# Kernel optimization log

Hardware: AMD Instinct MI355X
Metric: run time of the kernel (lower is better)

The kernel has to match this reference:

```python
import jax, jax.numpy as jnp
import numpy as np

N_QUBITS = 8  # 2**8 == hidden_dim == 256


def setup_inputs() -> dict:
    key = jax.random.key(0)
    ks = jax.random.split(key, 6)
    B, H, F = 131072, 256, 512
    s = lambda fan: 1.0 / np.sqrt(fan)
    return {
        "x": jax.random.normal(ks[0], (B, N_QUBITS), jnp.float32),
        "W1": jax.random.normal(ks[1], (N_QUBITS, H), jnp.float32) * s(N_QUBITS),
        "b1": jnp.zeros((H,), jnp.float32),
        "W2": jax.random.normal(ks[2], (H, H), jnp.float32) * s(H),
        "b2": jnp.zeros((H,), jnp.float32),
        "W3": jax.random.normal(ks[3], (H, H), jnp.float32) * s(H),
        "b3": jnp.zeros((H,), jnp.float32),
        "W4": jax.random.normal(ks[4], (H, F), jnp.float32) * s(H),
        "b4": jnp.zeros((F,), jnp.float32),
    }


def _quantum_state(enc):
    # Ry(theta_i) on qubit i from |0...0>: product state, amplitudes are
    # kron_i [cos(theta_i/2), sin(theta_i/2)] (real). Qubit 0 = most significant.
    half = enc[:, :N_QUBITS] * (jnp.pi / 2)  # theta/2 = enc*pi/2
    amps = jnp.stack([jnp.cos(half), jnp.sin(half)], axis=-1)  # [B, n, 2]
    B = enc.shape[0]
    state = jnp.ones((B, 1), enc.dtype)
    for i in range(N_QUBITS):  # fixed small structural loop
        state = (state[:, :, None] * amps[:, i, None, :]).reshape(B, -1)
    return state  # [B, 2**n]


def reference(x, W1, b1, W2, b2, W3, b3, W4, b4):
    h = jax.nn.relu(x @ W1 + b1)
    enc = jax.nn.relu(h @ W2 + b2)           # [B, 256]
    state = _quantum_state(enc)              # [B, 256]
    f = jax.nn.relu(state @ W3 + b3)
    return f @ W4 + b4                       # [B, 512]
```

## Files before the change

### kernel.cpp

```cpp
#include <hip/hip_runtime.h>
#include <hip/hip_bf16.h>

typedef short s8v __attribute__((ext_vector_type(8)));
typedef float f4v __attribute__((ext_vector_type(4)));
typedef unsigned short u16;
typedef unsigned int u32;

#define PI_HALF 1.57079632679489662f

__global__ void prep_kernel(const float* __restrict__ W1,
                            const float* __restrict__ W2,
                            const float* __restrict__ W3,
                            const float* __restrict__ W4,
                            u16* __restrict__ w3f,
                            u16* __restrict__ w4f,
                            float* __restrict__ w1t,
                            float* __restrict__ w2c) {
  int i = blockIdx.x * 256 + threadIdx.x;
  if (i < 65536) {
    int j = i & 7, lane = (i >> 3) & 63, kk = (i >> 9) & 7, ntg = i >> 12;
    int k = kk * 32 + (lane >> 4) * 8 + j;
    int n = ntg * 16 + (lane & 15);
    __hip_bfloat16 v = __float2bfloat16(W3[k * 256 + n]);
    w3f[i] = *(u16*)&v;
  } else if (i < 65536 + 131072) {
    int t = i - 65536;
    int j = t & 7, lane = (t >> 3) & 63, kk = (t >> 9) & 7, ntg = t >> 12;
    int k = kk * 32 + (lane >> 4) * 8 + j;
    int n = ntg * 16 + (lane & 15);
    __hip_bfloat16 v = __float2bfloat16(W4[k * 512 + n]);
    w4f[t] = *(u16*)&v;
  } else if (i < 65536 + 131072 + 2048) {
    int t = i - (65536 + 131072);
    int k = t >> 3, j = t & 7;
    w1t[t] = W1[j * 256 + k];
  } else if (i < 65536 + 131072 + 4096) {
    int t = i - (65536 + 131072 + 2048);
    int k = t >> 3, q = t & 7;
    w2c[t] = W2[k * 256 + q];
  }
}

__global__ void angle_kernel(const float* __restrict__ x,
                             const float* __restrict__ b1v,
                             const float* __restrict__ b2v,
                             const float* __restrict__ w1t,
                             const float* __restrict__ w2c,
                             float* __restrict__ cs, int B) {
  const int r = blockIdx.x * 256 + threadIdx.x;
  if (r >= B) return;
  float xv[8];
  {
    const float4* xp = (const float4*)(x + (size_t)r * 8);
    float4 a = xp[0], b = xp[1];
    xv[0] = a.x; xv[1] = a.y; xv[2] = a.z; xv[3] = a.w;
    xv[4] = b.x; xv[5] = b.y; xv[6] = b.z; xv[7] = b.w;
  }
  float e[8];
#pragma unroll
  for (int q = 0; q < 8; q++) e[q] = b2v[q];
#pragma unroll 4
  for (int k = 0; k < 256; k++) {
    const float4* wp = (const float4*)(w1t + k * 8);
    float4 wa = wp[0], wb = wp[1];
    float h = b1v[k];
    h = fmaf(xv[0], wa.x, h); h = fmaf(xv[1], wa.y, h);
    h = fmaf(xv[2], wa.z, h); h = fmaf(xv[3], wa.w, h);
    h = fmaf(xv[4], wb.x, h); h = fmaf(xv[5], wb.y, h);
    h = fmaf(xv[6], wb.z, h); h = fmaf(xv[7], wb.w, h);
    h = fmaxf(h, 0.f);
    const float4* w2p = (const float4*)(w2c + k * 8);
    float4 ya = w2p[0], yb = w2p[1];
    e[0] = fmaf(h, ya.x, e[0]); e[1] = fmaf(h, ya.y, e[1]);
    e[2] = fmaf(h, ya.z, e[2]); e[3] = fmaf(h, ya.w, e[3]);
    e[4] = fmaf(h, yb.x, e[4]); e[5] = fmaf(h, yb.y, e[5]);
    e[6] = fmaf(h, yb.z, e[6]); e[7] = fmaf(h, yb.w, e[7]);
  }
  float cc[8], ss[8];
#pragma unroll
  for (int q = 0; q < 8; q++) {
    float ang = fmaxf(e[q], 0.f) * PI_HALF;
    ss[q] = __sinf(ang);
    cc[q] = __cosf(ang);
  }
  float4* op = (float4*)(cs + (size_t)r * 16);
  op[0] = (float4){cc[0], cc[1], cc[2], cc[3]};
  op[1] = (float4){cc[4], cc[5], cc[6], cc[7]};
  op[2] = (float4){ss[0], ss[1], ss[2], ss[3]};
  op[3] = (float4){ss[4], ss[5], ss[6], ss[7]};
}

__global__ __launch_bounds__(512, 2)
void gemm_kernel(const float* __restrict__ cs,
                 const float* __restrict__ b3v,
                 const float* __restrict__ b4v,
                 const u16* __restrict__ w3f,
                 const u16* __restrict__ w4f,
                 float* __restrict__ out, int B) {
  __shared__ alignas(16) u16 st[64 * 256];
  const int tid = threadIdx.x;
  const int row0 = blockIdx.x * 64;

  {
    const int rl = tid >> 3;
    const int s  = tid & 7;
    const int r  = row0 + rl;
    float4 ca, cb, sa, sb;
    if (r < B) {
      const float4* ip = (const float4*)(cs + (size_t)r * 16);
      ca = ip[0]; cb = ip[1]; sa = ip[2]; sb = ip[3];
    } else {
      ca = cb = sa = sb = (float4){0.f, 0.f, 0.f, 0.f};
    }
    float q0 = (s & 4) ? sa.x : ca.x;
    float q1 = (s & 2) ? sa.y : ca.y;
    float q2 = (s & 1) ? sa.z : ca.z;
    float prefix = q0 * q1 * q2;
    float A2_0 = prefix * ca.w;
    float A2_1 = prefix * sa.w;
    float L16[16];
    {
      float t4[4], t8[8];
      t4[0] = cb.x * cb.y; t4[1] = cb.x * sb.y;
      t4[2] = sb.x * cb.y; t4[3] = sb.x * sb.y;
#pragma unroll
      for (int j = 0; j < 4; j++) { t8[2*j] = t4[j] * cb.z; t8[2*j+1] = t4[j] * sb.z; }
#pragma unroll
      for (int j = 0; j < 8; j++) { L16[2*j] = t8[j] * cb.w; L16[2*j+1] = t8[j] * sb.w; }
    }
#pragma unroll
    for (int it = 0; it < 4; it++) {
      float ah = (it < 2) ? A2_0 : A2_1;
      const int lo0 = (it & 1) << 3;
      union { u16 h8[8]; uint4 u4; } pk;
#pragma unroll
      for (int j = 0; j < 8; j++) {
        __hip_bfloat16 bv = __float2bfloat16(ah * L16[lo0 + j]);
        pk.h8[j] = *(u16*)&bv;
      }
      u32 byte = (u32)(rl * 512 + (s * 4 + it) * 16) ^ (u32)((rl & 7) << 4);
      *(uint4*)((char*)st + byte) = pk.u4;
    }
  }
  __syncthreads();

  const int lane = tid & 63;
  const int wid  = tid >> 6;
  const int wm   = wid >> 2;
  const int wn   = wid & 3;
  const int lr   = lane & 15;
  const int lg   = lane >> 4;
  const int m0   = wm * 32;

  f4v accA[4][2];
#pragma unroll
  for (int nt = 0; nt < 4; nt++)
#pragma unroll
    for (int mt = 0; mt < 2; mt++) accA[nt][mt] = (f4v){0.f, 0.f, 0.f, 0.f};

  for (int kk = 0; kk < 8; kk++) {
    s8v a[2];
#pragma unroll
    for (int mt = 0; mt < 2; mt++) {
      int row = m0 + mt * 16 + lr;
      u32 byte = (u32)(row * 512 + kk * 64 + lg * 16) ^ (u32)((row & 7) << 4);
      a[mt] = *(const s8v*)((const char*)st + byte);
    }
#pragma unroll
    for (int nt = 0; nt < 4; nt++) {
      int ntg = wn * 4 + nt;
      s8v b = ((const s8v*)w3f)[(ntg * 8 + kk) * 64 + lane];
#pragma unroll
      for (int mt = 0; mt < 2; mt++)
        accA[nt][mt] = __builtin_amdgcn_mfma_f32_16x16x32_bf16(a[mt], b, accA[nt][mt], 0, 0, 0);
    }
  }
  __syncthreads();

#pragma unroll
  for (int nt = 0; nt < 4; nt++) {
    int col = wn * 64 + nt * 16 + lr;
    float bias = b3v[col];
#pragma unroll
    for (int mt = 0; mt < 2; mt++) {
#pragma unroll
      for (int i = 0; i < 4; i++) {
        int row = m0 + mt * 16 + lg * 4 + i;
        float v = fmaxf(accA[nt][mt][i] + bias, 0.f);
        __hip_bfloat16 bv = __float2bfloat16(v);
        u32 byte = (u32)(row * 512 + col * 2) ^ (u32)((row & 7) << 4);
        *(u16*)((char*)st + byte) = *(u16*)&bv;
      }
    }
  }
  __syncthreads();

#pragma unroll 1
  for (int nh = 0; nh < 2; nh++) {
    const int nbase = wn * 128 + nh * 64;
    f4v accB[4][2];
#pragma unroll
    for (int nt = 0; nt < 4; nt++)
#pragma unroll
      for (int mt = 0; mt < 2; mt++) accB[nt][mt] = (f4v){0.f, 0.f, 0.f, 0.f};

    for (int kk = 0; kk < 8; kk++) {
      s8v a[2];
#pragma unroll
      for (int mt = 0; mt < 2; mt++) {
        int row = m0 + mt * 16 + lr;
        u32 byte = (u32)(row * 512 + kk * 64 + lg * 16) ^ (u32)((row & 7) << 4);
        a[mt] = *(const s8v*)((const char*)st + byte);
      }
#pragma unroll
      for (int nt = 0; nt < 4; nt++) {
        int ntg = (nbase >> 4) + nt;
        s8v b = ((const s8v*)w4f)[(ntg * 8 + kk) * 64 + lane];
#pragma unroll
        for (int mt = 0; mt < 2; mt++)
          accB[nt][mt] = __builtin_amdgcn_mfma_f32_16x16x32_bf16(a[mt], b, accB[nt][mt], 0, 0, 0);
      }
    }
#pragma unroll
    for (int nt = 0; nt < 4; nt++) {
      int col = nbase + nt * 16 + lr;
      float bias = b4v[col];
#pragma unroll
      for (int mt = 0; mt < 2; mt++) {
        int rowg = row0 + m0 + mt * 16 + lg * 4;
        if (rowg + 3 < B) {
          float* op = out + (size_t)rowg * 512 + col;
          op[0]    = accB[nt][mt][0] + bias;
          op[512]  = accB[nt][mt][1] + bias;
          op[1024] = accB[nt][mt][2] + bias;
          op[1536] = accB[nt][mt][3] + bias;
        } else {
#pragma unroll
          for (int i = 0; i < 4; i++)
            if (rowg + i < B) out[(size_t)(rowg + i) * 512 + col] = accB[nt][mt][i] + bias;
        }
      }
    }
  }
}

extern "C" void kernel_launch(void* const* d_in, const int* in_sizes, int n_in,
                              void* d_out, int out_size, void* d_ws, size_t ws_size,
                              hipStream_t stream) {
  const float* x  = (const float*)d_in[0];
  const float* W1 = (const float*)d_in[1];
  const float* b1 = (const float*)d_in[2];
  const float* W2 = (const float*)d_in[3];
  const float* b2 = (const float*)d_in[4];
  const float* W3 = (const float*)d_in[5];
  const float* b3 = (const float*)d_in[6];
  const float* W4 = (const float*)d_in[7];
  const float* b4 = (const float*)d_in[8];
  float* out = (float*)d_out;
  const int B = in_sizes[0] / 8;

  u16*   w3f = (u16*)d_ws;
  u16*   w4f = (u16*)((char*)d_ws + 131072);
  float* w1t = (float*)((char*)d_ws + 131072 + 262144);
  float* w2c = (float*)((char*)d_ws + 131072 + 262144 + 8192);
  float* cs  = (float*)((char*)d_ws + 131072 + 262144 + 16384);

  prep_kernel<<<784, 256, 0, stream>>>(W1, W2, W3, W4, w3f, w4f, w1t, w2c);
  angle_kernel<<<(B + 255) / 256, 256, 0, stream>>>(x, b1, b2, w1t, w2c, cs, B);
  gemm_kernel<<<(B + 63) / 64, 512, 0, stream>>>(cs, b3, b4, w3f, w4f, out, B);
}
```

Baseline: 201.3 us.

## Halve gemm block to 4 waves, each covering all 64 rows

The fused GEMM kernel now runs 256 threads (4 waves) per 64-row block instead of 512 (8 waves). Each wave covers all 64 rows and a 64-column slice, so every global B-fragment load of W3/W4 feeds four MFMAs instead of two, which halves weight traffic per output. State construction is redistributed so each thread writes 8 chunks of 8 amplitudes. The cost is twice the accumulator registers per thread and fewer waves to hide latency, with launch bounds (256,2) possibly limiting occupancy.

Result: faster. 181.4 us (median of 2 runs) (-9.9%).

```diff
diff --git a/kernel.cpp b/kernel.cpp
--- a/kernel.cpp
+++ b/kernel.cpp
@@ -90,7 +90,7 @@
   op[3] = (float4){ss[4], ss[5], ss[6], ss[7]};
 }
 
-__global__ __launch_bounds__(512, 2)
+__global__ __launch_bounds__(256, 2)
 void gemm_kernel(const float* __restrict__ cs,
                  const float* __restrict__ b3v,
                  const float* __restrict__ b4v,
@@ -102,8 +102,8 @@
   const int row0 = blockIdx.x * 64;
 
   {
-    const int rl = tid >> 3;
-    const int s  = tid & 7;
+    const int rl = tid >> 2;
+    const int s  = tid & 3;
     const int r  = row0 + rl;
     float4 ca, cb, sa, sb;
     if (r < B) {
@@ -112,57 +112,63 @@
     } else {
       ca = cb = sa = sb = (float4){0.f, 0.f, 0.f, 0.f};
     }
-    float q0 = (s & 4) ? sa.x : ca.x;
-    float q1 = (s & 2) ? sa.y : ca.y;
-    float q2 = (s & 1) ? sa.z : ca.z;
-    float prefix = q0 * q1 * q2;
-    float A2_0 = prefix * ca.w;
-    float A2_1 = prefix * sa.w;
-    float L16[16];
+    float q0 = (s & 2) ? sa.x : ca.x;
+    float q1 = (s & 1) ? sa.y : ca.y;
+    float p01 = q0 * q1;
+    float A8[8];
     {
-      float t4[4], t8[8];
-      t4[0] = cb.x * cb.y; t4[1] = cb.x * sb.y;
-      t4[2] = sb.x * cb.y; t4[3] = sb.x * sb.y;
-#pragma unroll
-      for (int j = 0; j < 4; j++) { t8[2*j] = t4[j] * cb.z; t8[2*j+1] = t4[j] * sb.z; }
-#pragma unroll
-      for (int j = 0; j < 8; j++) { L16[2*j] = t8[j] * cb.w; L16[2*j+1] = t8[j] * sb.w; }
-    }
-#pragma unroll
-    for (int it = 0; it < 4; it++) {
-      float ah = (it < 2) ? A2_0 : A2_1;
-      const int lo0 = (it & 1) << 3;
+      float c2 = ca.z, s2 = sa.z, c3 = ca.w, s3 = sa.w, c4 = cb.x, s4 = sb.x;
+      float p23[4];
+      p23[0] = c2 * c3; p23[1] = c2 * s3; p23[2] = s2 * c3; p23[3] = s2 * s3;
+#pragma unroll
+      for (int m = 0; m < 4; m++) {
+        A8[2*m]   = p01 * p23[m] * c4;
+        A8[2*m+1] = p01 * p23[m] * s4;
+      }
+    }
+    float L8[8];
+    {
+      float c5 = cb.y, s5 = sb.y, c6 = cb.z, s6 = sb.z, c7 = cb.w, s7 = sb.w;
+      float p56[4];
+      p56[0] = c5 * c6; p56[1] = c5 * s6; p56[2] = s5 * c6; p56[3] = s5 * s6;
+#pragma unroll
+      for (int m = 0; m < 4; m++) {
+        L8[2*m]   = p56[m] * c7;
+        L8[2*m+1] = p56[m] * s7;
+      }
+    }
+#pragma unroll
+    for (int it = 0; it < 8; it++) {
+      float ah = A8[it];
       union { u16 h8[8]; uint4 u4; } pk;
 #pragma unroll
       for (int j = 0; j < 8; j++) {
-        __hip_bfloat16 bv = __float2bfloat16(ah * L16[lo0 + j]);
+        __hip_bfloat16 bv = __float2bfloat16(ah * L8[j]);
         pk.h8[j] = *(u16*)&bv;
       }
-      u32 byte = (u32)(rl * 512 + (s * 4 + it) * 16) ^ (u32)((rl & 7) << 4);
+      u32 byte = (u32)(rl * 512 + (s * 8 + it) * 16) ^ (u32)((rl & 7) << 4);
       *(uint4*)((char*)st + byte) = pk.u4;
     }
   }
   __syncthreads();
 
   const int lane = tid & 63;
-  const int wid  = tid >> 6;
-  const int wm   = wid >> 2;
-  const int wn   = wid & 3;
+  const int wn   = tid >> 6;
   const int lr   = lane & 15;
   const int lg   = lane >> 4;
-  const int m0   = wm * 32;
-
-  f4v accA[4][2];
+
+  f4v acc[4][4];
+
 #pragma unroll
   for (int nt = 0; nt < 4; nt++)
 #pragma unroll
-    for (int mt = 0; mt < 2; mt++) accA[nt][mt] = (f4v){0.f, 0.f, 0.f, 0.f};
+    for (int mt = 0; mt < 4; mt++) acc[nt][mt] = (f4v){0.f, 0.f, 0.f, 0.f};
 
   for (int kk = 0; kk < 8; kk++) {
-    s8v a[2];
-#pragma unroll
-    for (int mt = 0; mt < 2; mt++) {
-      int row = m0 + mt * 16 + lr;
+    s8v a[4];
+#pragma unroll
+    for (int mt = 0; mt < 4; mt++) {
+      int row = mt * 16 + lr;
       u32 byte = (u32)(row * 512 + kk * 64 + lg * 16) ^ (u32)((row & 7) << 4);
       a[mt] = *(const s8v*)((const char*)st + byte);
     }
@@ -171,8 +177,8 @@
       int ntg = wn * 4 + nt;
       s8v b = ((const s8v*)w3f)[(ntg * 8 + kk) * 64 + lane];
 #pragma unroll
-      for (int mt = 0; mt < 2; mt++)
-        accA[nt][mt] = __builtin_amdgcn_mfma_f32_16x16x32_bf16(a[mt], b, accA[nt][mt], 0, 0, 0);
+      for (int mt = 0; mt < 4; mt++)
+        acc[nt][mt] = __builtin_amdgcn_mfma_f32_16x16x32_bf16(a[mt], b, acc[nt][mt], 0, 0, 0);
     }
   }
   __syncthreads();
@@ -182,11 +188,11 @@
     int col = wn * 64 + nt * 16 + lr;
     float bias = b3v[col];
 #pragma unroll
-    for (int mt = 0; mt < 2; mt++) {
+    for (int mt = 0; mt < 4; mt++) {
 #pragma unroll
       for (int i = 0; i < 4; i++) {
-        int row = m0 + mt * 16 + lg * 4 + i;
-        float v = fmaxf(accA[nt][mt][i] + bias, 0.f);
+        int row = mt * 16 + lg * 4 + i;
+        float v = fmaxf(acc[nt][mt][i] + bias, 0.f);
         __hip_bfloat16 bv = __float2bfloat16(v);
         u32 byte = (u32)(row * 512 + col * 2) ^ (u32)((row & 7) << 4);
         *(u16*)((char*)st + byte) = *(u16*)&bv;
@@ -198,17 +204,16 @@
 #pragma unroll 1
   for (int nh = 0; nh < 2; nh++) {
     const int nbase = wn * 128 + nh * 64;
-    f4v accB[4][2];
 #pragma unroll
     for (int nt = 0; nt < 4; nt++)
 #pragma unroll
-      for (int mt = 0; mt < 2; mt++) accB[nt][mt] = (f4v){0.f, 0.f, 0.f, 0.f};
+      for (int mt = 0; mt < 4; mt++) acc[nt][mt] = (f4v){0.f, 0.f, 0.f, 0.f};
 
     for (int kk = 0; kk < 8; kk++) {
-      s8v a[2];
-#pragma unroll
-      for (int mt = 0; mt < 2; mt++) {
-        int row = m0 + mt * 16 + lr;
+      s8v a[4];
+#pragma unroll
+      for (int mt = 0; mt < 4; mt++) {
+        int row = mt * 16 + lr;
         u32 byte = (u32)(row * 512 + kk * 64 + lg * 16) ^ (u32)((row & 7) << 4);
         a[mt] = *(const s8v*)((const char*)st + byte);
       }
@@ -217,8 +222,8 @@
         int ntg = (nbase >> 4) + nt;
         s8v b = ((const s8v*)w4f)[(ntg * 8 + kk) * 64 + lane];
 #pragma unroll
-        for (int mt = 0; mt < 2; mt++)
-          accB[nt][mt] = __builtin_amdgcn_mfma_f32_16x16x32_bf16(a[mt], b, accB[nt][mt], 0, 0, 0);
+        for (int mt = 0; mt < 4; mt++)
+          acc[nt][mt] = __builtin_amdgcn_mfma_f32_16x16x32_bf16(a[mt], b, acc[nt][mt], 0, 0, 0);
       }
     }
 #pragma unroll
@@ -226,18 +231,18 @@
       int col = nbase + nt * 16 + lr;
       float bias = b4v[col];
 #pragma unroll
-      for (int mt = 0; mt < 2; mt++) {
-        int rowg = row0 + m0 + mt * 16 + lg * 4;
+      for (int mt = 0; mt < 4; mt++) {
+        int rowg = row0 + mt * 16 + lg * 4;
         if (rowg + 3 < B) {
           float* op = out + (size_t)rowg * 512 + col;
-          op[0]    = accB[nt][mt][0] + bias;
-          op[512]  = accB[nt][mt][1] + bias;
-          op[1024] = accB[nt][mt][2] + bias;
-          op[1536] = accB[nt][mt][3] + bias;
+          op[0]    = acc[nt][mt][0] + bias;
+          op[512]  = acc[nt][mt][1] + bias;
+          op[1024] = acc[nt][mt][2] + bias;
+          op[1536] = acc[nt][mt][3] + bias;
         } else {
 #pragma unroll
           for (int i = 0; i < 4; i++)
-            if (rowg + i < B) out[(size_t)(rowg + i) * 512 + col] = accB[nt][mt][i] + bias;
+            if (rowg + i < B) out[(size_t)(rowg + i) * 512 + col] = acc[nt][mt][i] + bias;
         }
       }
     }
@@ -267,5 +272,5 @@
 
   prep_kernel<<<784, 256, 0, stream>>>(W1, W2, W3, W4, w3f, w4f, w1t, w2c);
   angle_kernel<<<(B + 255) / 256, 256, 0, stream>>>(x, b1, b2, w1t, w2c, cs, B);
-  gemm_kernel<<<(B + 63) / 64, 512, 0, stream>>>(cs, b3, b4, w3f, w4f, out, B);
-}
+  gemm_kernel<<<(B + 63) / 64, 256, 0, stream>>>(cs, b3, b4, w3f, w4f, out, B);
+}
```
